# Kernel optimization log

Hardware: AMD Instinct MI355X
Metric: run time of the kernel (lower is better)

The kernel has to match this reference:

```python
import jax, jax.numpy as jnp
import numpy as np

B, S, D_IN = 4, 2048, 1024
EMBED, HEADS = 1024, 16
HEAD_DIM = EMBED // HEADS


def setup_inputs() -> dict:
    key = jax.random.key(0)
    k1, k2, k3 = jax.random.split(key, 3)
    x = jax.random.normal(k1, (B, S, D_IN), dtype=jnp.float32)
    # xavier-uniform-ish init scales
    lim_qkv = float(np.sqrt(6.0 / (D_IN + 3 * EMBED)))
    lim_o = float(np.sqrt(6.0 / (EMBED + EMBED)))
    w_qkv = jax.random.uniform(k2, (3 * EMBED, D_IN), minval=-lim_qkv, maxval=lim_qkv, dtype=jnp.float32)
    b_qkv = jnp.zeros((3 * EMBED,), dtype=jnp.float32)
    w_o = jax.random.uniform(k3, (EMBED, EMBED), minval=-lim_o, maxval=lim_o, dtype=jnp.float32)
    b_o = jnp.zeros((EMBED,), dtype=jnp.float32)
    return {"x": x, "w_qkv": w_qkv, "b_qkv": b_qkv, "w_o": w_o, "b_o": b_o}


def reference(x, w_qkv, b_qkv, w_o, b_o):
    b, s, _ = x.shape
    qkv = jnp.einsum('bsi,oi->bso', x, w_qkv) + b_qkv            # (b, s, 3E)
    qkv = qkv.reshape(b, s, HEADS, 3 * HEAD_DIM).transpose(0, 2, 1, 3)  # (b, h, s, 3d)
    q, k, v = jnp.split(qkv, 3, axis=-1)                          # each (b, h, s, d)
    scale = 1.0 / jnp.sqrt(jnp.float32(HEAD_DIM))
    attn = jnp.einsum('bhqd,bhkd->bhqk', q, k) * scale            # (b, h, s, s)
    attn = jax.nn.softmax(attn, axis=-1)
    vals = jnp.einsum('bhqk,bhkd->bhqd', attn, v)                 # (b, h, s, d)
    # NOTE: original torch code reshapes (b,h,s,d) -> (b,s,e) WITHOUT transposing
    # heads back; jnp.reshape reproduces that flattening exactly.
    vals = vals.reshape(b, s, EMBED)
    out = jnp.einsum('bse,oe->bso', vals, w_o) + b_o              # (b, s, E)
    return out
```

## Files before the change

### kernel.cpp

```cpp
#include <hip/hip_runtime.h>
#include <stdint.h>
#include <stddef.h>

#define DEVINL __device__ __forceinline__

typedef unsigned short u16;
typedef unsigned int u32;
typedef __attribute__((ext_vector_type(8))) short short8;
typedef __attribute__((ext_vector_type(4))) float f32x4;
typedef __attribute__((ext_vector_type(4))) u32 u32x4;
typedef __attribute__((ext_vector_type(2))) u32 u32x2;

#define QSCALE 0.18033688011112042f

DEVINL u16 f2bf(float f) {
    u32 u = __builtin_bit_cast(u32, f);
    u32 r = (u + 0x7fffu + ((u >> 16) & 1u)) >> 16;
    return (u16)r;
}

DEVINL void gld_lds16(const void* g, void* l) {
    __builtin_amdgcn_global_load_lds(
        (__attribute__((address_space(1))) u32*)(uintptr_t)g,
        (__attribute__((address_space(3))) u32*)l, 16, 0, 0);
}

DEVINL u32 pack_bf16_trunc(float lo, float hi) {
    return __builtin_amdgcn_perm(__builtin_bit_cast(u32, hi),
                                 __builtin_bit_cast(u32, lo), 0x07060302u);
}

DEVINL void plswap32(u32 &a, u32 &b) {
#if __has_builtin(__builtin_amdgcn_permlane32_swap)
    u32x2 r = __builtin_amdgcn_permlane32_swap(a, b, false, false);
    a = r[0]; b = r[1];
#else
    asm("v_permlane32_swap_b32 %0, %1" : "+v"(a), "+v"(b));
#endif
}
DEVINL void plswap16(u32 &a, u32 &b) {
#if __has_builtin(__builtin_amdgcn_permlane16_swap)
    u32x2 r = __builtin_amdgcn_permlane16_swap(a, b, false, false);
    a = r[0]; b = r[1];
#else
    asm("v_permlane16_swap_b32 %0, %1" : "+v"(a), "+v"(b));
#endif
}

__global__ void prep_inputs(const float* __restrict__ x, const float* __restrict__ wqkv,
                            const float* __restrict__ bqkv, const float* __restrict__ wo,
                            u16* __restrict__ xb, u16* __restrict__ wqb,
                            u16* __restrict__ wob, float* __restrict__ bsc) {
    int blk = blockIdx.x;
    if (blk < 6144) {
        const float* src; u16* dst; int base; bool qscale = false;
        if (blk < 4096)      { src = x;    dst = xb;  base = blk; }
        else if (blk < 5632) { src = wqkv; dst = wqb; base = blk - 4096; qscale = true; }
        else                 { src = wo;   dst = wob; base = blk - 5632; }
        int i = (base * 256 + threadIdx.x) * 8;
        float sc = 1.0f;
        if (qscale) { int row = i >> 10; if ((row % 192) < 64) sc = QSCALE; }
        float4 a = *(const float4*)(src + i);
        float4 c = *(const float4*)(src + i + 4);
        union { u16 s[8]; u32x4 v; } t;
        t.s[0] = f2bf(a.x * sc); t.s[1] = f2bf(a.y * sc); t.s[2] = f2bf(a.z * sc); t.s[3] = f2bf(a.w * sc);
        t.s[4] = f2bf(c.x * sc); t.s[5] = f2bf(c.y * sc); t.s[6] = f2bf(c.z * sc); t.s[7] = f2bf(c.w * sc);
        *(u32x4*)(dst + i) = t.v;
    } else {
        int i = (blk - 6144) * 256 + threadIdx.x;
        float sc = ((i % 192) < 64) ? QSCALE : 1.0f;
        bsc[i] = bqkv[i] * sc;
    }
}

__global__ void gemm_qkv(const u16* __restrict__ A, const u16* __restrict__ Bm,
                         const float* __restrict__ bias, u16* __restrict__ qkvb,
                         u16* __restrict__ vtb) {
    const int K = 1024, N = 3072;
    __shared__ u16 As[128 * 64];
    __shared__ u16 Bs[128 * 64];
    const int tid = threadIdx.x;
    const int lane = tid & 63;
    const int wv = tid >> 6, wr = wv >> 1, wc = wv & 1;
    const int l15 = lane & 15, quad = lane >> 4;
    const int e7 = (l15 & 7) * 8;
    const int id = blockIdx.x;
    const int xcd = id & 7, rr = id >> 3;
    const int m0 = ((xcd << 3) + rr / 24) * 128;
    const int n0 = (rr % 24) * 128;

    f32x4 acc[4][4];
#pragma unroll
    for (int i = 0; i < 4; i++)
#pragma unroll
        for (int j = 0; j < 4; j++) acc[i][j] = (f32x4){0.f, 0.f, 0.f, 0.f};

    const u16* Ab = A + (size_t)m0 * K;
    const u16* Bb = Bm + (size_t)n0 * K;
    const int lrow = lane >> 3;
    const int lgr  = (lane & 7) ^ lrow;
    const int r0   = wv * 8 + lrow;

    for (int k0 = 0; k0 < K; k0 += 64) {
#pragma unroll
        for (int j = 0; j < 4; j++) {
            int row = j * 32 + r0;
            gld_lds16(Ab + (size_t)row * K + k0 + lgr * 8, (char*)As + (size_t)(j * 256 + tid) * 16);
            gld_lds16(Bb + (size_t)row * K + k0 + lgr * 8, (char*)Bs + (size_t)(j * 256 + tid) * 16);
        }
        __syncthreads();
#pragma unroll
        for (int ks = 0; ks < 2; ks++) {
            short8 af[4], bf8[4];
#pragma unroll
            for (int mi = 0; mi < 4; mi++)
                af[mi] = *(const short8*)(As + (wr * 64 + mi * 16 + l15) * 64 + ((ks * 32 + quad * 8) ^ e7));
#pragma unroll
            for (int ni = 0; ni < 4; ni++)
                bf8[ni] = *(const short8*)(Bs + (wc * 64 + ni * 16 + l15) * 64 + ((ks * 32 + quad * 8) ^ e7));
#pragma unroll
            for (int mi = 0; mi < 4; mi++)
#pragma unroll
                for (int ni = 0; ni < 4; ni++)
                    acc[mi][ni] = __builtin_amdgcn_mfma_f32_16x16x32_bf16(af[mi], bf8[ni], acc[mi][ni], 0, 0, 0);
        }
        __syncthreads();
    }

#pragma unroll
    for (int mi = 0; mi < 4; mi++) {
        int row_b = m0 + wr * 64 + mi * 16 + quad * 4;
#pragma unroll
        for (int ni = 0; ni < 4; ni++) {
            int c0 = n0 + wc * 64 + ni * 16;
            int sec0 = c0 % 192;
            float bv = bias[c0 + l15];
            float v0 = acc[mi][ni][0] + bv;
            float v1 = acc[mi][ni][1] + bv;
            float v2 = acc[mi][ni][2] + bv;
            float v3 = acc[mi][ni][3] + bv;
            if (sec0 >= 128) {
                int hh = c0 / 192;
                int b = row_b >> 11;
                int s = row_b & 2047;
                int d = sec0 - 128 + l15;
                u32 lo = (u32)f2bf(v0) | ((u32)f2bf(v1) << 16);
                u32 hi = (u32)f2bf(v2) | ((u32)f2bf(v3) << 16);
                *(u32x2*)(vtb + ((size_t)((b * 16 + hh) * 64 + d)) * 2048 + s) = (u32x2){lo, hi};
            } else {
                int col = c0 + l15;
                qkvb[(size_t)(row_b + 0) * N + col] = f2bf(v0);
                qkvb[(size_t)(row_b + 1) * N + col] = f2bf(v1);
                qkvb[(size_t)(row_b + 2) * N + col] = f2bf(v2);
                qkvb[(size_t)(row_b + 3) * N + col] = f2bf(v3);
            }
        }
    }
}

__global__ void gemm_out(const u16* __restrict__ A, const u16* __restrict__ Bm,
                         const float* __restrict__ bias, float* __restrict__ C) {
    const int K = 1024, N = 1024;
    __shared__ u16 As[128 * 64];
    __shared__ u16 Bs[64 * 64];
    const int tid = threadIdx.x;
    const int lane = tid & 63;
    const int wv = tid >> 6, wr = wv >> 1, wc = wv & 1;
    const int l15 = lane & 15, quad = lane >> 4;
    const int e7 = (l15 & 7) * 8;
    const int id = blockIdx.x;
    const int xcd = id & 7, rr = id >> 3;
    const int m0 = ((xcd << 3) + (rr >> 4)) * 128;
    const int n0 = (rr & 15) * 64;

    f32x4 acc[4][2];
#pragma unroll
    for (int i = 0; i < 4; i++)
#pragma unroll
        for (int j = 0; j < 2; j++) acc[i][j] = (f32x4){0.f, 0.f, 0.f, 0.f};

    const u16* Ab = A + (size_t)m0 * K;
    const u16* Bb = Bm + (size_t)n0 * K;
    const int lrow = lane >> 3;
    const int lgr  = (lane & 7) ^ lrow;
    const int r0   = wv * 8 + lrow;

    for (int k0 = 0; k0 < K; k0 += 64) {
#pragma unroll
        for (int j = 0; j < 4; j++)
            gld_lds16(Ab + (size_t)(j * 32 + r0) * K + k0 + lgr * 8,
                      (char*)As + (size_t)(j * 256 + tid) * 16);
#pragma unroll
        for (int j = 0; j < 2; j++)
            gld_lds16(Bb + (size_t)(j * 32 + r0) * K + k0 + lgr * 8,
                      (char*)Bs + (size_t)(j * 256 + tid) * 16);
        __syncthreads();
#pragma unroll
        for (int ks = 0; ks < 2; ks++) {
            short8 af[4], bf8[2];
#pragma unroll
            for (int mi = 0; mi < 4; mi++)
                af[mi] = *(const short8*)(As + (wr * 64 + mi * 16 + l15) * 64 + ((ks * 32 + quad * 8) ^ e7));
#pragma unroll
            for (int ni = 0; ni < 2; ni++)
                bf8[ni] = *(const short8*)(Bs + (wc * 32 + ni * 16 + l15) * 64 + ((ks * 32 + quad * 8) ^ e7));
#pragma unroll
            for (int mi = 0; mi < 4; mi++)
#pragma unroll
                for (int ni = 0; ni < 2; ni++)
                    acc[mi][ni] = __builtin_amdgcn_mfma_f32_16x16x32_bf16(af[mi], bf8[ni], acc[mi][ni], 0, 0, 0);
        }
        __syncthreads();
    }

#pragma unroll
    for (int mi = 0; mi < 4; mi++) {
        int row_b = m0 + wr * 64 + mi * 16 + quad * 4;
#pragma unroll
        for (int ni = 0; ni < 2; ni++) {
            int col = n0 + wc * 32 + ni * 16 + l15;
            float bv = bias[col];
#pragma unroll
            for (int r = 0; r < 4; r++)
                C[(size_t)(row_b + r) * N + col] = acc[mi][ni][r] + bv;
        }
    }
}

__launch_bounds__(256, 4)
__global__ void flash_attn(const u16* __restrict__ qkv, const u16* __restrict__ vt,
                           u16* __restrict__ vals2) {
    __shared__ u16 Ks[2][64 * 64];
    __shared__ u16 Vts[2][64 * 64];

    const int tid = threadIdx.x;
    const int lane = tid & 63, wv = tid >> 6;
    const int l15 = lane & 15, quad = lane >> 4;
    const int e7 = (l15 & 7) * 8;
    const int id = blockIdx.x;
    const int m = id >> 3;
    const int bh = ((id & 7) << 3) + (m >> 4);
    const int s0 = (m & 15) << 7;
    const int b = bh >> 4, h = bh & 15;

    short8 qf[2][2];
    const u16* qbase = qkv + (size_t)(b * 2048 + s0 + wv * 32) * 3072 + h * 192;
#pragma unroll
    for (int qi = 0; qi < 2; qi++)
#pragma unroll
        for (int ks = 0; ks < 2; ks++)
            qf[qi][ks] = *(const short8*)(qbase + (size_t)(qi * 16 + l15) * 3072 + ks * 32 + quad * 8);

    f32x4 o_acc[2][4];
    f32x4 sum_acc[2];
#pragma unroll
    for (int qi = 0; qi < 2; qi++) {
        sum_acc[qi] = (f32x4){0.f, 0.f, 0.f, 0.f};
#pragma unroll
        for (int nd = 0; nd < 4; nd++) o_acc[qi][nd] = (f32x4){0.f, 0.f, 0.f, 0.f};
    }

    const u16* kg = qkv + (size_t)(b * 2048) * 3072 + h * 192 + 64;
    const u16* vg = vt + (size_t)bh * 64 * 2048;

    const int lrow = lane >> 3;
    const int lgr  = (lane & 7) ^ lrow;
    const int r0   = wv * 8 + lrow;

    const short8 ones = (short8){0x3F80, 0x3F80, 0x3F80, 0x3F80, 0x3F80, 0x3F80, 0x3F80, 0x3F80};

#pragma unroll
    for (int j = 0; j < 2; j++) {
        int row = j * 32 + r0;
        gld_lds16(kg + (size_t)row * 3072 + lgr * 8, (char*)&Ks[0][0] + (size_t)(j * 256 + tid) * 16);
        gld_lds16(vg + (size_t)row * 2048 + lgr * 8, (char*)&Vts[0][0] + (size_t)(j * 256 + tid) * 16);
    }
    __syncthreads();

    int cur = 0;
    for (int kb = 0; kb < 2048; kb += 64) {
        if (kb + 64 < 2048) {
            int nb = cur ^ 1;
#pragma unroll
            for (int j = 0; j < 2; j++) {
                int row = j * 32 + r0;
                gld_lds16(kg + (size_t)(kb + 64 + row) * 3072 + lgr * 8,
                          (char*)&Ks[nb][0] + (size_t)(j * 256 + tid) * 16);
                gld_lds16(vg + (size_t)row * 2048 + kb + 64 + lgr * 8,
                          (char*)&Vts[nb][0] + (size_t)(j * 256 + tid) * 16);
            }
        }

        f32x4 s_acc[4][2];
#pragma unroll
        for (int ki = 0; ki < 4; ki++)
#pragma unroll
            for (int qi = 0; qi < 2; qi++) s_acc[ki][qi] = (f32x4){0.f, 0.f, 0.f, 0.f};
        __builtin_amdgcn_s_setprio(1);
#pragma unroll
        for (int ki = 0; ki < 4; ki++) {
#pragma unroll
            for (int ks = 0; ks < 2; ks++) {
                short8 kf = *(const short8*)(&Ks[cur][0] + (ki * 16 + l15) * 64 + ((ks * 32 + quad * 8) ^ e7));
#pragma unroll
                for (int qi = 0; qi < 2; qi++)
                    s_acc[ki][qi] = __builtin_amdgcn_mfma_f32_16x16x32_bf16(kf, qf[qi][ks], s_acc[ki][qi], 0, 0, 0);
            }
        }
        __builtin_amdgcn_s_setprio(0);

        short8 ap[2][2];
#pragma unroll
        for (int c = 0; c < 2; c++)
#pragma unroll
            for (int qi = 0; qi < 2; qi++) {
                u32 w0 = pack_bf16_trunc(__builtin_amdgcn_exp2f(s_acc[2 * c][qi][0]),
                                         __builtin_amdgcn_exp2f(s_acc[2 * c][qi][1]));
                u32 w1 = pack_bf16_trunc(__builtin_amdgcn_exp2f(s_acc[2 * c][qi][2]),
                                         __builtin_amdgcn_exp2f(s_acc[2 * c][qi][3]));
                u32 w2 = pack_bf16_trunc(__builtin_amdgcn_exp2f(s_acc[2 * c + 1][qi][0]),
                                         __builtin_amdgcn_exp2f(s_acc[2 * c + 1][qi][1]));
                u32 w3 = pack_bf16_trunc(__builtin_amdgcn_exp2f(s_acc[2 * c + 1][qi][2]),
                                         __builtin_amdgcn_exp2f(s_acc[2 * c + 1][qi][3]));
                plswap32(w0, w2);
                plswap32(w1, w3);
                plswap16(w0, w2);
                plswap16(w1, w3);
                u32x4 wf = (u32x4){w0, w1, w2, w3};
                ap[qi][c] = __builtin_bit_cast(short8, wf);
            }

#pragma unroll
        for (int c = 0; c < 2; c++) {
#pragma unroll
            for (int qi = 0; qi < 2; qi++)
                sum_acc[qi] = __builtin_amdgcn_mfma_f32_16x16x32_bf16(ap[qi][c], ones, sum_acc[qi], 0, 0, 0);
            __builtin_amdgcn_s_setprio(1);
#pragma unroll
            for (int nd = 0; nd < 4; nd++) {
                short8 bv = *(const short8*)(&Vts[cur][0] + (nd * 16 + l15) * 64 + ((c * 32 + quad * 8) ^ e7));
#pragma unroll
                for (int qi = 0; qi < 2; qi++)
                    o_acc[qi][nd] = __builtin_amdgcn_mfma_f32_16x16x32_bf16(ap[qi][c], bv, o_acc[qi][nd], 0, 0, 0);
            }
            __builtin_amdgcn_s_setprio(0);
        }

        __syncthreads();
        cur ^= 1;
    }

#pragma unroll
    for (int qi = 0; qi < 2; qi++) {
        f32x4 inv;
#pragma unroll
        for (int r = 0; r < 4; r++) inv[r] = 1.0f / sum_acc[qi][r];
#pragma unroll
        for (int nd = 0; nd < 4; nd++) {
            int d = nd * 16 + l15;
#pragma unroll
            for (int r = 0; r < 4; r++) {
                int s = s0 + wv * 32 + qi * 16 + quad * 4 + r;
                size_t row2 = (size_t)(b * 2048 + h * 128 + (s >> 4));
                int col2 = ((s & 15) << 6) + d;
                vals2[row2 * 1024 + col2] = f2bf(o_acc[qi][nd][r] * inv[r]);
            }
        }
    }
}

extern "C" void kernel_launch(void* const* d_in, const int* in_sizes, int n_in,
                              void* d_out, int out_size, void* d_ws, size_t ws_size,
                              hipStream_t stream) {
    (void)in_sizes; (void)n_in; (void)out_size; (void)ws_size;
    const float* x      = (const float*)d_in[0];
    const float* w_qkv  = (const float*)d_in[1];
    const float* b_qkv  = (const float*)d_in[2];
    const float* w_o    = (const float*)d_in[3];
    const float* b_o    = (const float*)d_in[4];
    float* out = (float*)d_out;

    char* ws = (char*)d_ws;
    u16* xb   = (u16*)(ws);
    u16* wqb  = (u16*)(ws + 16777216);
    u16* wob  = (u16*)(ws + 23068672);
    u16* qkvb = (u16*)(ws + 25165824);
    u16* vtb  = (u16*)(ws + 75497472);
    u16* v2b  = (u16*)(ws + 92274688);
    float* bsc = (float*)(ws + 92274688);

    prep_inputs<<<6156, 256, 0, stream>>>(x, w_qkv, b_qkv, w_o, xb, wqb, wob, bsc);

    gemm_qkv<<<1536, 256, 0, stream>>>(xb, wqb, bsc, qkvb, vtb);

    flash_attn<<<1024, 256, 0, stream>>>(qkvb, vtb, v2b);

    gemm_out<<<1024, 256, 0, stream>>>(v2b, wob, b_o, out);
}
```

Measured before the change: 241.7 us.

## Use 512-thread attention blocks covering 256 queries to share K/V tiles

The flash attention kernel now launches 512 blocks of 512 threads (8 waves) instead of 1024 blocks of 256, so each block handles 256 query rows. Each thread issues one K and one V LDS load per tile instead of two, halving redundant K/V global traffic per query. The S-tile MFMA chain also starts from a zero constant instead of explicitly zeroing accumulators. The larger blocks raise register and occupancy pressure under the 512,4 launch bound, which may limit waves per CU.

```diff
diff --git a/kernel.cpp b/kernel.cpp
--- a/kernel.cpp
+++ b/kernel.cpp
@@ -227,7 +227,7 @@
     }
 }
 
-__launch_bounds__(256, 4)
+__launch_bounds__(512, 4)
 __global__ void flash_attn(const u16* __restrict__ qkv, const u16* __restrict__ vt,
                            u16* __restrict__ vals2) {
     __shared__ u16 Ks[2][64 * 64];
@@ -239,8 +239,8 @@
     const int e7 = (l15 & 7) * 8;
     const int id = blockIdx.x;
     const int m = id >> 3;
-    const int bh = ((id & 7) << 3) + (m >> 4);
-    const int s0 = (m & 15) << 7;
+    const int bh = ((id & 7) << 3) + (m >> 3);
+    const int s0 = (m & 7) << 8;
     const int b = bh >> 4, h = bh & 15;
 
     short8 qf[2][2];
@@ -259,6 +259,7 @@
 #pragma unroll
         for (int nd = 0; nd < 4; nd++) o_acc[qi][nd] = (f32x4){0.f, 0.f, 0.f, 0.f};
     }
+    const f32x4 fzero = (f32x4){0.f, 0.f, 0.f, 0.f};
 
     const u16* kg = qkv + (size_t)(b * 2048) * 3072 + h * 192 + 64;
     const u16* vg = vt + (size_t)bh * 64 * 2048;
@@ -269,43 +270,32 @@
 
     const short8 ones = (short8){0x3F80, 0x3F80, 0x3F80, 0x3F80, 0x3F80, 0x3F80, 0x3F80, 0x3F80};
 
-#pragma unroll
-    for (int j = 0; j < 2; j++) {
-        int row = j * 32 + r0;
-        gld_lds16(kg + (size_t)row * 3072 + lgr * 8, (char*)&Ks[0][0] + (size_t)(j * 256 + tid) * 16);
-        gld_lds16(vg + (size_t)row * 2048 + lgr * 8, (char*)&Vts[0][0] + (size_t)(j * 256 + tid) * 16);
-    }
+    gld_lds16(kg + (size_t)r0 * 3072 + lgr * 8, (char*)&Ks[0][0] + (size_t)tid * 16);
+    gld_lds16(vg + (size_t)r0 * 2048 + lgr * 8, (char*)&Vts[0][0] + (size_t)tid * 16);
     __syncthreads();
 
     int cur = 0;
     for (int kb = 0; kb < 2048; kb += 64) {
         if (kb + 64 < 2048) {
             int nb = cur ^ 1;
-#pragma unroll
-            for (int j = 0; j < 2; j++) {
-                int row = j * 32 + r0;
-                gld_lds16(kg + (size_t)(kb + 64 + row) * 3072 + lgr * 8,
-                          (char*)&Ks[nb][0] + (size_t)(j * 256 + tid) * 16);
-                gld_lds16(vg + (size_t)row * 2048 + kb + 64 + lgr * 8,
-                          (char*)&Vts[nb][0] + (size_t)(j * 256 + tid) * 16);
-            }
+            gld_lds16(kg + (size_t)(kb + 64 + r0) * 3072 + lgr * 8,
+                      (char*)&Ks[nb][0] + (size_t)tid * 16);
+            gld_lds16(vg + (size_t)r0 * 2048 + kb + 64 + lgr * 8,
+                      (char*)&Vts[nb][0] + (size_t)tid * 16);
         }
 
         f32x4 s_acc[4][2];
-#pragma unroll
-        for (int ki = 0; ki < 4; ki++)
-#pragma unroll
-            for (int qi = 0; qi < 2; qi++) s_acc[ki][qi] = (f32x4){0.f, 0.f, 0.f, 0.f};
         __builtin_amdgcn_s_setprio(1);
 #pragma unroll
         for (int ki = 0; ki < 4; ki++) {
-#pragma unroll
-            for (int ks = 0; ks < 2; ks++) {
-                short8 kf = *(const short8*)(&Ks[cur][0] + (ki * 16 + l15) * 64 + ((ks * 32 + quad * 8) ^ e7));
-#pragma unroll
-                for (int qi = 0; qi < 2; qi++)
-                    s_acc[ki][qi] = __builtin_amdgcn_mfma_f32_16x16x32_bf16(kf, qf[qi][ks], s_acc[ki][qi], 0, 0, 0);
-            }
+            short8 kf0 = *(const short8*)(&Ks[cur][0] + (ki * 16 + l15) * 64 + ((quad * 8) ^ e7));
+            short8 kf1 = *(const short8*)(&Ks[cur][0] + (ki * 16 + l15) * 64 + ((32 + quad * 8) ^ e7));
+#pragma unroll
+            for (int qi = 0; qi < 2; qi++)
+                s_acc[ki][qi] = __builtin_amdgcn_mfma_f32_16x16x32_bf16(kf0, qf[qi][0], fzero, 0, 0, 0);
+#pragma unroll
+            for (int qi = 0; qi < 2; qi++)
+                s_acc[ki][qi] = __builtin_amdgcn_mfma_f32_16x16x32_bf16(kf1, qf[qi][1], s_acc[ki][qi], 0, 0, 0);
         }
         __builtin_amdgcn_s_setprio(0);
 
@@ -393,7 +383,7 @@
 
     gemm_qkv<<<1536, 256, 0, stream>>>(xb, wqb, bsc, qkvb, vtb);
 
-    flash_attn<<<1024, 256, 0, stream>>>(qkvb, vtb, v2b);
+    flash_attn<<<512, 512, 0, stream>>>(qkvb, vtb, v2b);
 
     gemm_out<<<1024, 256, 0, stream>>>(v2b, wob, b_o, out);
 }
```

Measured after the change: 242.4 us. No clear change (+0.3%).
